# Performance work log

Hardware: AMD Instinct MI355X
Metric: run time of the kernel (lower is better)

The kernel has to match this reference:

```python
import jax, jax.numpy as jnp
import numpy as np

EMB_DIM = 1024
H = 16
HEAD_DIM = EMB_DIM // H
B = 2
S = 2048  # enc and dec seq len
LN_EPS = 1e-5


def setup_inputs() -> dict:
    key = jax.random.key(0)
    ks = jax.random.split(key, 8)
    scale_in = 1.0 / np.sqrt(EMB_DIM)
    scale_o = 1.0 / np.sqrt(H * HEAD_DIM)
    return {
        "enc_out": jax.random.normal(ks[0], (B, S, EMB_DIM), jnp.float32),
        "dec_out": jax.random.normal(ks[1], (B, S, EMB_DIM), jnp.float32),
        # stacked per-head projections, equivalent to h separate Linear(emb_dim, head_dim, bias=False)
        "Wq": jax.random.uniform(ks[2], (H, EMB_DIM, HEAD_DIM), jnp.float32, -scale_in, scale_in),
        "Wk": jax.random.uniform(ks[3], (H, EMB_DIM, HEAD_DIM), jnp.float32, -scale_in, scale_in),
        "Wv": jax.random.uniform(ks[4], (H, EMB_DIM, HEAD_DIM), jnp.float32, -scale_in, scale_in),
        "Wo": jax.random.uniform(ks[5], (H * HEAD_DIM, EMB_DIM), jnp.float32, -scale_o, scale_o),
        "gamma": jnp.ones((EMB_DIM,), jnp.float32),
        "beta": jnp.zeros((EMB_DIM,), jnp.float32),
    }


def reference(enc_out, dec_out, Wq, Wk, Wv, Wo, gamma, beta):
    d = Wq.shape[-1]
    # per-head projections, batched over heads (same math as the Python loop)
    q = jnp.einsum('bse,hed->bhsd', dec_out, Wq)   # queries from decoder
    k = jnp.einsum('bte,hed->bhtd', enc_out, Wk)   # keys from encoder
    v = jnp.einsum('bte,hed->bhtd', enc_out, Wv)   # values from encoder
    scores = jnp.einsum('bhsd,bhtd->bhst', q, k) / jnp.sqrt(jnp.asarray(d, q.dtype))
    att = jax.nn.softmax(scores, axis=-1)
    ctx = jnp.einsum('bhst,bhtd->bhsd', att, v)
    b, h, s, hd = ctx.shape
    ctx = ctx.transpose(0, 2, 1, 3).reshape(b, s, h * hd)  # concat heads along feature dim
    transformed = ctx @ Wo  # dropout is identity in eval mode
    x = dec_out + transformed
    mu = jnp.mean(x, axis=-1, keepdims=True)
    var = jnp.mean(jnp.square(x - mu), axis=-1, keepdims=True)
    return (x - mu) * jax.lax.rsqrt(var + LN_EPS) * gamma + beta
```

## Files before the change

kernel.cpp:

```cpp
#include <hip/hip_runtime.h>
#include <hip/hip_bf16.h>

#define EMB   1024
#define NH    16
#define HD    64
#define SEQ   2048
#define SA    72

typedef __attribute__((ext_vector_type(8))) short          bf16x8;
typedef __attribute__((ext_vector_type(8))) unsigned short us8;
typedef __attribute__((ext_vector_type(4))) float          f32x4;

__device__ __forceinline__ float u2f(unsigned short u) {
    return __uint_as_float(((unsigned)u) << 16);
}
__device__ __forceinline__ unsigned short f2u(float f) {
    __hip_bfloat16 b = __float2bfloat16(f);
    return *reinterpret_cast<unsigned short*>(&b);
}
__device__ __forceinline__ bool detect_bf16(const void* gamma) {
    return ((const unsigned short*)gamma)[0] == 0x3F80;
}
__device__ __forceinline__ f32x4 fzero() {
    f32x4 v; v.x = v.y = v.z = v.w = 0.f; return v;
}
__device__ __forceinline__ void ld16f(const void* p, size_t idx, bool isbf, float* o) {
    if (isbf) {
        const unsigned short* b = (const unsigned short*)p + idx;
        us8 v0 = *(const us8*)b, v1 = *(const us8*)(b + 8);
        #pragma unroll
        for (int i = 0; i < 8; ++i) { o[i] = u2f(v0[i]); o[8 + i] = u2f(v1[i]); }
    } else {
        const float* f = (const float*)p + idx;
        #pragma unroll
        for (int i = 0; i < 4; ++i) {
            float4 v = *(const float4*)(f + 4 * i);
            o[4*i] = v.x; o[4*i+1] = v.y; o[4*i+2] = v.z; o[4*i+3] = v.w;
        }
    }
}
__device__ __forceinline__ float ld1f(const void* p, size_t i, bool isbf) {
    return isbf ? u2f(((const unsigned short*)p)[i]) : ((const float*)p)[i];
}
__device__ __forceinline__ float4 ld4(const void* p, size_t idx, bool isbf) {
    if (isbf) {
        ushort4 t = *reinterpret_cast<const ushort4*>((const unsigned short*)p + idx);
        return make_float4(u2f(t.x), u2f(t.y), u2f(t.z), u2f(t.w));
    }
    return *reinterpret_cast<const float4*>((const float*)p + idx);
}
__device__ __forceinline__ us8 pk8(const float* s) {
    us8 v;
    #pragma unroll
    for (int i = 0; i < 8; ++i) v[i] = f2u(s[i]);
    return v;
}
__device__ __forceinline__ f32x4 mfma16(bf16x8 a, bf16x8 b, f32x4 c) {
    return __builtin_amdgcn_mfma_f32_16x16x32_bf16(a, b, c, 0, 0, 0);
}
__device__ __forceinline__ bf16x8 mk8(unsigned w0, unsigned w1, unsigned w2, unsigned w3) {
    union { unsigned u[4]; bf16x8 v; } x;
    x.u[0] = w0; x.u[1] = w1; x.u[2] = w2; x.u[3] = w3;
    return x.v;
}
__device__ __forceinline__ void gl_lds16(const unsigned short* g, unsigned short* l) {
    __builtin_amdgcn_global_load_lds(
        (const __attribute__((address_space(1))) void*)g,
        (__attribute__((address_space(3))) void*)l,
        16, 0, 0);
}

#define QSCALE 0.18033688f

__global__ __launch_bounds__(256) void convert_x_kernel(
    const void* __restrict__ dec, const void* __restrict__ enc,
    const void* __restrict__ gamma, unsigned short* __restrict__ xb)
{
    const bool isbf = detect_bf16(gamma);
    const size_t HALF = (size_t)4096 * 1024;
    size_t idx = ((size_t)blockIdx.x * 256 + threadIdx.x) * 16;
    const void* src; size_t off;
    if (idx < HALF) { src = dec; off = idx; } else { src = enc; off = idx - HALF; }
    float buf[16];
    ld16f(src, off, isbf, buf);
    *(us8*)&xb[idx]     = pk8(buf);
    *(us8*)&xb[idx + 8] = pk8(buf + 8);
}

__global__ __launch_bounds__(256) void transpose_w_kernel(
    const void* __restrict__ Wq, const void* __restrict__ Wk,
    const void* __restrict__ Wv, const void* __restrict__ gamma,
    unsigned short* __restrict__ wt)
{
    const bool isbf = detect_bf16(gamma);
    const int which = blockIdx.z, h = blockIdx.y, e0 = blockIdx.x * 64;
    const void* W = (which == 0) ? Wq : (which == 1 ? Wk : Wv);

    __shared__ unsigned short T[64][SA];
    const int sr = threadIdx.x >> 2, sc = (threadIdx.x & 3) * 16;

    float buf[16];
    ld16f(W, ((size_t)h * EMB + e0 + sr) * HD + sc, isbf, buf);
    #pragma unroll
    for (int i = 0; i < 16; ++i) T[sc + i][sr] = f2u(buf[i]);
    __syncthreads();
    us8 v0 = *(const us8*)&T[sr][sc];
    us8 v1 = *(const us8*)&T[sr][sc + 8];
    size_t o = (((size_t)which * NH + h) * HD + sr) * EMB + e0 + sc;
    *(us8*)&wt[o] = v0;
    *(us8*)&wt[o + 8] = v1;
}

__global__ __launch_bounds__(256) void transpose_wo_kernel(
    const void* __restrict__ Wo, const void* __restrict__ gamma,
    unsigned short* __restrict__ wot)
{
    const bool isbf = detect_bf16(gamma);
    const int n0 = blockIdx.x * 64, k0 = blockIdx.y * 64;
    __shared__ unsigned short T[64][SA];
    const int sr = threadIdx.x >> 2, sc = (threadIdx.x & 3) * 16;

    float buf[16];
    ld16f(Wo, (size_t)(k0 + sr) * EMB + n0 + sc, isbf, buf);
    #pragma unroll
    for (int i = 0; i < 16; ++i) T[sc + i][sr] = f2u(buf[i]);
    __syncthreads();
    us8 v0 = *(const us8*)&T[sr][sc];
    us8 v1 = *(const us8*)&T[sr][sc + 8];
    size_t o = (size_t)(n0 + sr) * EMB + k0 + sc;
    *(us8*)&wot[o] = v0;
    *(us8*)&wot[o + 8] = v1;
}

__global__ __launch_bounds__(256) void qkv_kernel(
    const unsigned short* __restrict__ xb,
    const unsigned short* __restrict__ wt,
    unsigned short* __restrict__ qo, unsigned short* __restrict__ ko,
    unsigned short* __restrict__ vt)
{
    const int id = blockIdx.x;
    const int xcd = id & 7, sl = id >> 3;
    const int m_t = xcd * 4 + (sl & 3);
    const int n_t = sl >> 2;
    const int m0 = m_t * 128, n0g = n_t * 128;
    const int which = n0g >> 10;
    const int nloc = n0g & 1023;
    const unsigned short* X = xb + ((which == 0) ? (size_t)0 : (size_t)4096 * 1024);

    __shared__ unsigned short smem[17408];
    unsigned short* const ldsA = smem;
    unsigned short* const ldsB = smem + 8192;

    const int tid = threadIdx.x, wv = tid >> 6, lane = tid & 63;
    const int lq = lane >> 4, lm = lane & 15;
    const int mw = (wv & 1) * 64, nw = (wv >> 1) * 64;

    const unsigned short* Wb = wt + (size_t)(which * 1024 + nloc) * EMB;

    const int seg0 = wv * 4;
    const int srow = lane >> 3;
    const int su   = (lane & 7) ^ srow;
    const unsigned short* aP[4];
    const unsigned short* bP[4];
    #pragma unroll
    for (int q = 0; q < 4; ++q) {
        const int s = seg0 + q;
        aP[q] = X  + (size_t)(m0 + 8 * s + srow) * EMB + su * 8;
        bP[q] = Wb + (size_t)(8 * s + srow) * EMB + su * 8;
    }

    f32x4 acc[4][4];
    #pragma unroll
    for (int i = 0; i < 4; ++i)
        #pragma unroll
        for (int j = 0; j < 4; ++j) acc[i][j] = fzero();

    const int xa = lm & 7;

    for (int k0 = 0; k0 < EMB; k0 += 64) {
        #pragma unroll
        for (int q = 0; q < 4; ++q) {
            gl_lds16(aP[q] + k0, ldsA + (seg0 + q) * 512);
            gl_lds16(bP[q] + k0, ldsB + (seg0 + q) * 512);
        }
        asm volatile("s_waitcnt vmcnt(0)" ::: "memory");
        __syncthreads();

        #pragma unroll
        for (int st = 0; st < 2; ++st) {
            const int u = (st * 4 + lq) ^ xa;
            bf16x8 af[4], bq[4];
            #pragma unroll
            for (int i = 0; i < 4; ++i)
                af[i] = *(const bf16x8*)(ldsA + (mw + i * 16 + lm) * 64 + u * 8);
            #pragma unroll
            for (int j = 0; j < 4; ++j)
                bq[j] = *(const bf16x8*)(ldsB + (nw + j * 16 + lm) * 64 + u * 8);
            #pragma unroll
            for (int i = 0; i < 4; ++i)
                #pragma unroll
                for (int j = 0; j < 4; ++j)
                    acc[i][j] = mfma16(af[i], bq[j], acc[i][j]);
        }
        __syncthreads();
    }

    const int b = m0 >> 11, s0 = m0 & (SEQ - 1);
    const float osc = (which == 0) ? QSCALE : 1.0f;
    if (which != 2) {
        unsigned short* Y = which ? ko : qo;
        #pragma unroll
        for (int i = 0; i < 4; ++i)
            #pragma unroll
            for (int j = 0; j < 4; ++j)
                #pragma unroll
                for (int r = 0; r < 4; ++r) {
                    int m = mw + i * 16 + lq * 4 + r;
                    int n = nloc + nw + j * 16 + lm;
                    int h = n >> 6, d = n & 63;
                    Y[(((size_t)b * NH + h) * SEQ + s0 + m) * HD + d] = f2u(acc[i][j][r] * osc);
                }
    } else {
        __syncthreads();
        unsigned short* vbuf = smem;
        #pragma unroll
        for (int i = 0; i < 4; ++i)
            #pragma unroll
            for (int j = 0; j < 4; ++j) {
                ushort4 p;
                p.x = f2u(acc[i][j][0]); p.y = f2u(acc[i][j][1]);
                p.z = f2u(acc[i][j][2]); p.w = f2u(acc[i][j][3]);
                *(ushort4*)&vbuf[(size_t)(nw + j * 16 + lm) * 136 + mw + i * 16 + lq * 4] = p;
            }
        __syncthreads();
        const int dd = tid >> 1, cc = (tid & 1) * 64;
        const int n = nloc + dd, h = n >> 6, d = n & 63;
        size_t o = (((size_t)b * NH + h) * HD + d) * SEQ + s0 + cc;
        #pragma unroll
        for (int jj = 0; jj < 8; ++jj)
            *(us8*)&vt[o + 8 * jj] = *(const us8*)&vbuf[(size_t)dd * 136 + cc + 8 * jj];
    }
}

__global__ __launch_bounds__(256) void attn_kernel(
    const unsigned short* __restrict__ qg,
    const unsigned short* __restrict__ kg,
    const unsigned short* __restrict__ vtg,
    unsigned short* __restrict__ ctx)
{
    __shared__ unsigned short Ks[2][4096];
    __shared__ unsigned short Vt[2][4096];

    const int tid = threadIdx.x, wv = tid >> 6, lane = tid & 63;
    const int lq = lane >> 4, lm = lane & 15;
    const int bh = blockIdx.x, q0 = blockIdx.y * 64;
    const unsigned short* Kg = kg + (size_t)bh * SEQ * HD;
    const unsigned short* Vg = vtg + (size_t)bh * HD * SEQ;

    const int srow = lane >> 3;
    const int su   = (lane & 7) ^ srow;
    const unsigned short* kS0 = Kg + (size_t)(8 * wv       + srow) * HD  + su * 8;
    const unsigned short* kS1 = Kg + (size_t)(8 * (wv + 4) + srow) * HD  + su * 8;
    const unsigned short* vS0 = Vg + (size_t)(8 * wv       + srow) * SEQ + su * 8;
    const unsigned short* vS1 = Vg + (size_t)(8 * (wv + 4) + srow) * SEQ + su * 8;

    bf16x8 qf[2];
    #pragma unroll
    for (int st = 0; st < 2; ++st)
        qf[st] = *(const bf16x8*)(qg + (size_t)bh * SEQ * HD
                      + (size_t)(q0 + wv * 16 + lm) * HD + st * 32 + lq * 8);

    bf16x8 onesf;
    #pragma unroll
    for (int i = 0; i < 8; ++i) onesf[i] = (short)0x3F80;

    f32x4 Of[4], lacc = fzero();
    #pragma unroll
    for (int t = 0; t < 4; ++t) Of[t] = fzero();

    const int xa = lm & 7;

    {
        gl_lds16(kS0, &Ks[0][wv * 512]);
        gl_lds16(kS1, &Ks[0][(wv + 4) * 512]);
        gl_lds16(vS0, &Vt[0][wv * 512]);
        gl_lds16(vS1, &Vt[0][(wv + 4) * 512]);
    }

    for (int it = 0; it < SEQ / 64; ++it) {
        const int cur = it & 1;
        if (it + 1 < SEQ / 64) {
            const size_t ko = (size_t)(it + 1) * 64 * HD;
            const int    vo = (it + 1) * 64;
            gl_lds16(kS0 + ko, &Ks[cur ^ 1][wv * 512]);
            gl_lds16(kS1 + ko, &Ks[cur ^ 1][(wv + 4) * 512]);
            gl_lds16(vS0 + vo, &Vt[cur ^ 1][wv * 512]);
            gl_lds16(vS1 + vo, &Vt[cur ^ 1][(wv + 4) * 512]);
            asm volatile("s_waitcnt vmcnt(4)" ::: "memory");
        } else {
            asm volatile("s_waitcnt vmcnt(0)" ::: "memory");
        }
        __syncthreads();

        f32x4 sf[4];
        #pragma unroll
        for (int t = 0; t < 4; ++t) sf[t] = fzero();
        __builtin_amdgcn_s_setprio(1);
        #pragma unroll
        for (int st = 0; st < 2; ++st) {
            const int u = (st * 4 + lq) ^ xa;
            #pragma unroll
            for (int tt = 0; tt < 4; ++tt) {
                bf16x8 kf = *(const bf16x8*)&Ks[cur][(lm + 16 * tt) * 64 + u * 8];
                sf[tt] = mfma16(kf, qf[st], sf[tt]);
            }
        }
        __builtin_amdgcn_s_setprio(0);

        unsigned pw[4][2];
        #pragma unroll
        for (int tt = 0; tt < 4; ++tt) {
            float p0 = exp2f(sf[tt][0]);
            float p1 = exp2f(sf[tt][1]);
            float p2 = exp2f(sf[tt][2]);
            float p3 = exp2f(sf[tt][3]);
            pw[tt][0] = (unsigned)f2u(p0) | ((unsigned)f2u(p1) << 16);
            pw[tt][1] = (unsigned)f2u(p2) | ((unsigned)f2u(p3) << 16);
        }
        #pragma unroll
        for (int a = 0; a < 2; ++a)
            #pragma unroll
            for (int c = 0; c < 2; ++c)
                asm("v_permlane32_swap_b32 %0, %1"
                    : "+v"(pw[2 * a][c]), "+v"(pw[2 * a + 1][c]));
        #pragma unroll
        for (int a = 0; a < 2; ++a)
            #pragma unroll
            for (int c = 0; c < 2; ++c)
                asm("v_permlane16_swap_b32 %0, %1"
                    : "+v"(pw[2 * a][c]), "+v"(pw[2 * a + 1][c]));

        __builtin_amdgcn_s_setprio(1);
        #pragma unroll
        for (int st = 0; st < 2; ++st) {
            const int u = (st * 4 + lq) ^ xa;
            bf16x8 pf = mk8(pw[2 * st][0], pw[2 * st][1],
                            pw[2 * st + 1][0], pw[2 * st + 1][1]);
            #pragma unroll
            for (int t = 0; t < 4; ++t) {
                bf16x8 vf = *(const bf16x8*)&Vt[cur][(lm + 16 * t) * 64 + u * 8];
                Of[t] = mfma16(pf, vf, Of[t]);
            }
            lacc = mfma16(pf, onesf, lacc);
        }
        __builtin_amdgcn_s_setprio(0);
        __syncthreads();
    }

    const int b = bh >> 4, h = bh & 15;
    #pragma unroll
    for (int r = 0; r < 4; ++r) {
        float inv = 1.0f / lacc[r];
        int srow2 = q0 + wv * 16 + lq * 4 + r;
        #pragma unroll
        for (int t = 0; t < 4; ++t) {
            int d = lm + 16 * t;
            ctx[((size_t)b * SEQ + srow2) * EMB + h * HD + d] = f2u(Of[t][r] * inv);
        }
    }
}

__global__ __launch_bounds__(256) void oproj_kernel(
    const unsigned short* __restrict__ ctx,
    const unsigned short* __restrict__ wot,
    const void* __restrict__ dec, const void* __restrict__ gamma,
    float* __restrict__ x)
{
    const bool isbf = detect_bf16(gamma);
    const int id = blockIdx.x;
    const int xcd = id & 7, sl = id >> 3;
    const int m0 = (xcd * 4 + (sl & 3)) * 128;
    const int n0 = (sl >> 2) * 128;

    __shared__ unsigned short smem[16384];
    unsigned short* const ldsA = smem;
    unsigned short* const ldsB = smem + 8192;

    const int tid = threadIdx.x, wv = tid >> 6, lane = tid & 63;
    const int lq = lane >> 4, lm = lane & 15;
    const int mw = (wv & 1) * 64, nw = (wv >> 1) * 64;

    const int seg0 = wv * 4;
    const int srow = lane >> 3;
    const int su   = (lane & 7) ^ srow;
    const unsigned short* aP[4];
    const unsigned short* bP[4];
    #pragma unroll
    for (int q = 0; q < 4; ++q) {
        const int s = seg0 + q;
        aP[q] = ctx + (size_t)(m0 + 8 * s + srow) * EMB + su * 8;
        bP[q] = wot + (size_t)(n0 + 8 * s + srow) * EMB + su * 8;
    }

    f32x4 acc[4][4];
    #pragma unroll
    for (int i = 0; i < 4; ++i)
        #pragma unroll
        for (int j = 0; j < 4; ++j) acc[i][j] = fzero();

    const int xa = lm & 7;

    for (int k0 = 0; k0 < EMB; k0 += 64) {
        #pragma unroll
        for (int q = 0; q < 4; ++q) {
            gl_lds16(aP[q] + k0, ldsA + (seg0 + q) * 512);
            gl_lds16(bP[q] + k0, ldsB + (seg0 + q) * 512);
        }
        asm volatile("s_waitcnt vmcnt(0)" ::: "memory");
        __syncthreads();

        #pragma unroll
        for (int st = 0; st < 2; ++st) {
            const int u = (st * 4 + lq) ^ xa;
            bf16x8 af[4], bq[4];
            #pragma unroll
            for (int i = 0; i < 4; ++i)
                af[i] = *(const bf16x8*)(ldsA + (mw + i * 16 + lm) * 64 + u * 8);
            #pragma unroll
            for (int j = 0; j < 4; ++j)
                bq[j] = *(const bf16x8*)(ldsB + (nw + j * 16 + lm) * 64 + u * 8);
            #pragma unroll
            for (int i = 0; i < 4; ++i)
                #pragma unroll
                for (int j = 0; j < 4; ++j)
                    acc[i][j] = mfma16(af[i], bq[j], acc[i][j]);
        }
        __syncthreads();
    }

    #pragma unroll
    for (int i = 0; i < 4; ++i)
        #pragma unroll
        for (int j = 0; j < 4; ++j)
            #pragma unroll
            for (int r = 0; r < 4; ++r) {
                int m = m0 + mw + i * 16 + lq * 4 + r;
                int n = n0 + nw + j * 16 + lm;
                x[(size_t)m * EMB + n] = acc[i][j][r] + ld1f(dec, (size_t)m * EMB + n, isbf);
            }
}

__global__ __launch_bounds__(256) void ln_kernel(
    const float* __restrict__ x,
    const void* __restrict__ gamma,
    const void* __restrict__ beta,
    void* __restrict__ out)
{
    const bool isbf = detect_bf16(gamma);
    const int row = blockIdx.x;
    const int tid = threadIdx.x;
    const float* xr = x + (size_t)row * EMB;

    float4 xv = *reinterpret_cast<const float4*>(&xr[tid * 4]);
    float s1 = xv.x + xv.y + xv.z + xv.w;
    float s2 = xv.x * xv.x + xv.y * xv.y + xv.z * xv.z + xv.w * xv.w;

    #pragma unroll
    for (int off = 32; off > 0; off >>= 1) {
        s1 += __shfl_down(s1, off);
        s2 += __shfl_down(s2, off);
    }
    __shared__ float w1[4], w2[4];
    const int wid = tid >> 6, lane = tid & 63;
    if (lane == 0) { w1[wid] = s1; w2[wid] = s2; }
    __syncthreads();
    s1 = w1[0] + w1[1] + w1[2] + w1[3];
    s2 = w2[0] + w2[1] + w2[2] + w2[3];

    const float mu  = s1 * (1.0f / EMB);
    const float var = s2 * (1.0f / EMB) - mu * mu;
    const float rs  = rsqrtf(var + 1e-5f);

    float4 gv = ld4(gamma, (size_t)tid * 4, isbf);
    float4 bv = ld4(beta,  (size_t)tid * 4, isbf);
    float4 r;
    r.x = (xv.x - mu) * rs * gv.x + bv.x;
    r.y = (xv.y - mu) * rs * gv.y + bv.y;
    r.z = (xv.z - mu) * rs * gv.z + bv.z;
    r.w = (xv.w - mu) * rs * gv.w + bv.w;

    size_t o = (size_t)row * EMB + tid * 4;
    if (isbf) {
        ushort4 w;
        w.x = f2u(r.x); w.y = f2u(r.y); w.z = f2u(r.z); w.w = f2u(r.w);
        *reinterpret_cast<ushort4*>((unsigned short*)out + o) = w;
    } else {
        *reinterpret_cast<float4*>((float*)out + o) = r;
    }
}

extern "C" void kernel_launch(void* const* d_in, const int* in_sizes, int n_in,
                              void* d_out, int out_size, void* d_ws, size_t ws_size,
                              hipStream_t stream)
{
    const void* enc   = d_in[0];
    const void* dec   = d_in[1];
    const void* Wq    = d_in[2];
    const void* Wk    = d_in[3];
    const void* Wv    = d_in[4];
    const void* Wo    = d_in[5];
    const void* gamma = d_in[6];
    const void* beta  = d_in[7];

    char* w = (char*)d_ws;
    unsigned short* qws  = (unsigned short*)(w);
    unsigned short* kws  = (unsigned short*)(w + (size_t)8  * 1024 * 1024);
    unsigned short* vtws = (unsigned short*)(w + (size_t)16 * 1024 * 1024);
    unsigned short* wotw = (unsigned short*)(w + (size_t)16 * 1024 * 1024);
    unsigned short* wtws = (unsigned short*)(w + (size_t)24 * 1024 * 1024);
    unsigned short* cws  = (unsigned short*)(w + (size_t)24 * 1024 * 1024);
    float*          xws  = (float*)         (w);
    unsigned short* xbuf = (unsigned short*)d_out;

    convert_x_kernel   <<<2048,            256, 0, stream>>>(dec, enc, gamma, xbuf);
    transpose_w_kernel <<<dim3(16, 16, 3), 256, 0, stream>>>(Wq, Wk, Wv, gamma, wtws);
    qkv_kernel         <<<768,             256, 0, stream>>>(xbuf, wtws, qws, kws, vtws);
    attn_kernel        <<<dim3(32, 32),    256, 0, stream>>>(qws, kws, vtws, cws);
    transpose_wo_kernel<<<dim3(16, 16),    256, 0, stream>>>(Wo, gamma, wotw);
    oproj_kernel       <<<256,             256, 0, stream>>>(cws, wotw, dec, gamma, xws);
    ln_kernel          <<<4096,            256, 0, stream>>>(xws, gamma, beta, d_out);
}
```

Baseline: 263.3 us.

## Give each attention wave two query tiles and use native exp2/bf16 pack

The attention kernel moves from 4 waves with 16 query rows each to 2 waves with 32 query rows each, so every K and V fragment read from LDS feeds two MFMAs instead of one. Each wave now issues more of the global-to-LDS loads, and the wait count is raised to match. Softmax exponentials use the hardware exp2 builtin, and pairs are packed to bf16 with v_cvt_pk_bf16_f32. The cost is fewer waves per block and higher register pressure, which may lower occupancy or latency hiding.

```diff
diff --git a/kernel.cpp b/kernel.cpp
--- a/kernel.cpp
+++ b/kernel.cpp
@@ -62,6 +62,14 @@
     union { unsigned u[4]; bf16x8 v; } x;
     x.u[0] = w0; x.u[1] = w1; x.u[2] = w2; x.u[3] = w3;
     return x.v;
+}
+__device__ __forceinline__ float fexp2(float x) {
+    return __builtin_amdgcn_exp2f(x);
+}
+__device__ __forceinline__ unsigned cvtpk(float lo, float hi) {
+    unsigned r;
+    asm("v_cvt_pk_bf16_f32 %0, %1, %2" : "=v"(r) : "v"(lo), "v"(hi));
+    return r;
 }
 __device__ __forceinline__ void gl_lds16(const unsigned short* g, unsigned short* l) {
     __builtin_amdgcn_global_load_lds(
@@ -242,7 +250,7 @@
     }
 }
 
-__global__ __launch_bounds__(256) void attn_kernel(
+__global__ __launch_bounds__(128) void attn_kernel(
     const unsigned short* __restrict__ qg,
     const unsigned short* __restrict__ kg,
     const unsigned short* __restrict__ vtg,
@@ -259,32 +267,41 @@
 
     const int srow = lane >> 3;
     const int su   = (lane & 7) ^ srow;
-    const unsigned short* kS0 = Kg + (size_t)(8 * wv       + srow) * HD  + su * 8;
-    const unsigned short* kS1 = Kg + (size_t)(8 * (wv + 4) + srow) * HD  + su * 8;
-    const unsigned short* vS0 = Vg + (size_t)(8 * wv       + srow) * SEQ + su * 8;
-    const unsigned short* vS1 = Vg + (size_t)(8 * (wv + 4) + srow) * SEQ + su * 8;
-
-    bf16x8 qf[2];
-    #pragma unroll
-    for (int st = 0; st < 2; ++st)
-        qf[st] = *(const bf16x8*)(qg + (size_t)bh * SEQ * HD
-                      + (size_t)(q0 + wv * 16 + lm) * HD + st * 32 + lq * 8);
+    const unsigned short* kSp[4];
+    const unsigned short* vSp[4];
+    #pragma unroll
+    for (int j = 0; j < 4; ++j) {
+        const int seg = wv + 2 * j;
+        kSp[j] = Kg + (size_t)(8 * seg + srow) * HD  + su * 8;
+        vSp[j] = Vg + (size_t)(8 * seg + srow) * SEQ + su * 8;
+    }
+
+    bf16x8 qf[2][2];
+    #pragma unroll
+    for (int s = 0; s < 2; ++s)
+        #pragma unroll
+        for (int st = 0; st < 2; ++st)
+            qf[s][st] = *(const bf16x8*)(qg + (size_t)bh * SEQ * HD
+                          + (size_t)(q0 + wv * 32 + s * 16 + lm) * HD + st * 32 + lq * 8);
 
     bf16x8 onesf;
     #pragma unroll
     for (int i = 0; i < 8; ++i) onesf[i] = (short)0x3F80;
 
-    f32x4 Of[4], lacc = fzero();
-    #pragma unroll
-    for (int t = 0; t < 4; ++t) Of[t] = fzero();
+    f32x4 Of[2][4], lacc[2];
+    #pragma unroll
+    for (int s = 0; s < 2; ++s) {
+        lacc[s] = fzero();
+        #pragma unroll
+        for (int t = 0; t < 4; ++t) Of[s][t] = fzero();
+    }
 
     const int xa = lm & 7;
 
-    {
-        gl_lds16(kS0, &Ks[0][wv * 512]);
-        gl_lds16(kS1, &Ks[0][(wv + 4) * 512]);
-        gl_lds16(vS0, &Vt[0][wv * 512]);
-        gl_lds16(vS1, &Vt[0][(wv + 4) * 512]);
+    #pragma unroll
+    for (int j = 0; j < 4; ++j) {
+        gl_lds16(kSp[j], &Ks[0][(wv + 2 * j) * 512]);
+        gl_lds16(vSp[j], &Vt[0][(wv + 2 * j) * 512]);
     }
 
     for (int it = 0; it < SEQ / 64; ++it) {
@@ -292,19 +309,22 @@
         if (it + 1 < SEQ / 64) {
             const size_t ko = (size_t)(it + 1) * 64 * HD;
             const int    vo = (it + 1) * 64;
-            gl_lds16(kS0 + ko, &Ks[cur ^ 1][wv * 512]);
-            gl_lds16(kS1 + ko, &Ks[cur ^ 1][(wv + 4) * 512]);
-            gl_lds16(vS0 + vo, &Vt[cur ^ 1][wv * 512]);
-            gl_lds16(vS1 + vo, &Vt[cur ^ 1][(wv + 4) * 512]);
-            asm volatile("s_waitcnt vmcnt(4)" ::: "memory");
+            #pragma unroll
+            for (int j = 0; j < 4; ++j) {
+                gl_lds16(kSp[j] + ko, &Ks[cur ^ 1][(wv + 2 * j) * 512]);
+                gl_lds16(vSp[j] + vo, &Vt[cur ^ 1][(wv + 2 * j) * 512]);
+            }
+            asm volatile("s_waitcnt vmcnt(8)" ::: "memory");
         } else {
             asm volatile("s_waitcnt vmcnt(0)" ::: "memory");
         }
         __syncthreads();
 
-        f32x4 sf[4];
-        #pragma unroll
-        for (int t = 0; t < 4; ++t) sf[t] = fzero();
+        f32x4 sf[2][4];
+        #pragma unroll
+        for (int s = 0; s < 2; ++s)
+            #pragma unroll
+            for (int t = 0; t < 4; ++t) sf[s][t] = fzero();
         __builtin_amdgcn_s_setprio(1);
         #pragma unroll
         for (int st = 0; st < 2; ++st) {
@@ -312,46 +332,53 @@
             #pragma unroll
             for (int tt = 0; tt < 4; ++tt) {
                 bf16x8 kf = *(const bf16x8*)&Ks[cur][(lm + 16 * tt) * 64 + u * 8];
-                sf[tt] = mfma16(kf, qf[st], sf[tt]);
+                sf[0][tt] = mfma16(kf, qf[0][st], sf[0][tt]);
+                sf[1][tt] = mfma16(kf, qf[1][st], sf[1][tt]);
             }
         }
         __builtin_amdgcn_s_setprio(0);
 
-        unsigned pw[4][2];
-        #pragma unroll
-        for (int tt = 0; tt < 4; ++tt) {
-            float p0 = exp2f(sf[tt][0]);
-            float p1 = exp2f(sf[tt][1]);
-            float p2 = exp2f(sf[tt][2]);
-            float p3 = exp2f(sf[tt][3]);
-            pw[tt][0] = (unsigned)f2u(p0) | ((unsigned)f2u(p1) << 16);
-            pw[tt][1] = (unsigned)f2u(p2) | ((unsigned)f2u(p3) << 16);
-        }
-        #pragma unroll
-        for (int a = 0; a < 2; ++a)
-            #pragma unroll
-            for (int c = 0; c < 2; ++c)
-                asm("v_permlane32_swap_b32 %0, %1"
-                    : "+v"(pw[2 * a][c]), "+v"(pw[2 * a + 1][c]));
-        #pragma unroll
-        for (int a = 0; a < 2; ++a)
-            #pragma unroll
-            for (int c = 0; c < 2; ++c)
-                asm("v_permlane16_swap_b32 %0, %1"
-                    : "+v"(pw[2 * a][c]), "+v"(pw[2 * a + 1][c]));
+        unsigned pw[2][4][2];
+        #pragma unroll
+        for (int s = 0; s < 2; ++s)
+            #pragma unroll
+            for (int tt = 0; tt < 4; ++tt) {
+                pw[s][tt][0] = cvtpk(fexp2(sf[s][tt][0]), fexp2(sf[s][tt][1]));
+                pw[s][tt][1] = cvtpk(fexp2(sf[s][tt][2]), fexp2(sf[s][tt][3]));
+            }
+        #pragma unroll
+        for (int s = 0; s < 2; ++s)
+            #pragma unroll
+            for (int a = 0; a < 2; ++a)
+                #pragma unroll
+                for (int c = 0; c < 2; ++c)
+                    asm("v_permlane32_swap_b32 %0, %1"
+                        : "+v"(pw[s][2 * a][c]), "+v"(pw[s][2 * a + 1][c]));
+        #pragma unroll
+        for (int s = 0; s < 2; ++s)
+            #pragma unroll
+            for (int a = 0; a < 2; ++a)
+                #pragma unroll
+                for (int c = 0; c < 2; ++c)
+                    asm("v_permlane16_swap_b32 %0, %1"
+                        : "+v"(pw[s][2 * a][c]), "+v"(pw[s][2 * a + 1][c]));
 
         __builtin_amdgcn_s_setprio(1);
         #pragma unroll
         for (int st = 0; st < 2; ++st) {
             const int u = (st * 4 + lq) ^ xa;
-            bf16x8 pf = mk8(pw[2 * st][0], pw[2 * st][1],
-                            pw[2 * st + 1][0], pw[2 * st + 1][1]);
+            bf16x8 pf0 = mk8(pw[0][2 * st][0], pw[0][2 * st][1],
+                             pw[0][2 * st + 1][0], pw[0][2 * st + 1][1]);
+            bf16x8 pf1 = mk8(pw[1][2 * st][0], pw[1][2 * st][1],
+                             pw[1][2 * st + 1][0], pw[1][2 * st + 1][1]);
             #pragma unroll
             for (int t = 0; t < 4; ++t) {
                 bf16x8 vf = *(const bf16x8*)&Vt[cur][(lm + 16 * t) * 64 + u * 8];
-                Of[t] = mfma16(pf, vf, Of[t]);
-            }
-            lacc = mfma16(pf, onesf, lacc);
+                Of[0][t] = mfma16(pf0, vf, Of[0][t]);
+                Of[1][t] = mfma16(pf1, vf, Of[1][t]);
+            }
+            lacc[0] = mfma16(pf0, onesf, lacc[0]);
+            lacc[1] = mfma16(pf1, onesf, lacc[1]);
         }
         __builtin_amdgcn_s_setprio(0);
         __syncthreads();
@@ -359,15 +386,17 @@
 
     const int b = bh >> 4, h = bh & 15;
     #pragma unroll
-    for (int r = 0; r < 4; ++r) {
-        float inv = 1.0f / lacc[r];
-        int srow2 = q0 + wv * 16 + lq * 4 + r;
-        #pragma unroll
-        for (int t = 0; t < 4; ++t) {
-            int d = lm + 16 * t;
-            ctx[((size_t)b * SEQ + srow2) * EMB + h * HD + d] = f2u(Of[t][r] * inv);
-        }
-    }
+    for (int s = 0; s < 2; ++s)
+        #pragma unroll
+        for (int r = 0; r < 4; ++r) {
+            float inv = 1.0f / lacc[s][r];
+            int srow2 = q0 + wv * 32 + s * 16 + lq * 4 + r;
+            #pragma unroll
+            for (int t = 0; t < 4; ++t) {
+                int d = lm + 16 * t;
+                ctx[((size_t)b * SEQ + srow2) * EMB + h * HD + d] = f2u(Of[s][t][r] * inv);
+            }
+        }
 }
 
 __global__ __launch_bounds__(256) void oproj_kernel(
@@ -525,7 +554,7 @@
     convert_x_kernel   <<<2048,            256, 0, stream>>>(dec, enc, gamma, xbuf);
     transpose_w_kernel <<<dim3(16, 16, 3), 256, 0, stream>>>(Wq, Wk, Wv, gamma, wtws);
     qkv_kernel         <<<768,             256, 0, stream>>>(xbuf, wtws, qws, kws, vtws);
-    attn_kernel        <<<dim3(32, 32),    256, 0, stream>>>(qws, kws, vtws, cws);
+    attn_kernel        <<<dim3(32, 32),    128, 0, stream>>>(qws, kws, vtws, cws);
     transpose_wo_kernel<<<dim3(16, 16),    256, 0, stream>>>(Wo, gamma, wotw);
     oproj_kernel       <<<256,             256, 0, stream>>>(cws, wotw, dec, gamma, xws);
     ln_kernel          <<<4096,            256, 0, stream>>>(xws, gamma, beta, d_out);
```

Measured after the change: 241.7 us. -8.2%, faster.
